# Kernel tuning notes

Hardware: AMD Instinct MI355X
Metric: run time of the kernel (lower is better)

The kernel has to match this reference:

```python
import jax, jax.numpy as jnp
import numpy as np

B, S, NX, H = 8, 1024, 1024, 16
HD = NX // H  # head dim = 64
MASKED_BIAS = -10000.0


def setup_inputs() -> dict:
    key = jax.random.key(0)
    ks = jax.random.split(key, 6)
    return {
        "x": jax.random.normal(ks[0], (B, S, NX), dtype=jnp.float32),
        "query": jax.random.normal(ks[1], (B, S, NX), dtype=jnp.float32),
        "c_attn_w": jax.random.normal(ks[2], (NX, 3 * NX), dtype=jnp.float32) * 0.02,
        "c_attn_b": jnp.zeros((3 * NX,), dtype=jnp.float32),
        "c_proj_w": jax.random.normal(ks[3], (NX, NX), dtype=jnp.float32) * 0.02,
        "c_proj_b": jnp.zeros((NX,), dtype=jnp.float32),
    }


def _split_heads(t):
    # [B, S, NX] -> [B, H, S, HD]
    b, s, _ = t.shape
    return t.reshape(b, s, H, HD).transpose(0, 2, 1, 3)


def reference(x, query, c_attn_w, c_attn_b, c_proj_w, c_proj_b):
    # Conv1D: y = x @ W + b
    kv = x @ c_attn_w + c_attn_b          # [B,S,3NX]; use key/value slices
    qy = query @ c_attn_w + c_attn_b      # [B,S,3NX]; use query slice
    q = _split_heads(qy[..., :NX])                     # [B,H,S,HD]
    k = _split_heads(kv[..., NX:2 * NX])               # [B,H,S,HD]
    v = _split_heads(kv[..., 2 * NX:])                 # [B,H,S,HD]

    w = jnp.einsum("bhqd,bhkd->bhqk", q, k) / jnp.sqrt(jnp.float32(HD))
    causal = jnp.tril(jnp.ones((S, S), dtype=bool))[None, None]
    w = jnp.where(causal, w, jnp.float32(MASKED_BIAS))
    w = jax.nn.softmax(w, axis=-1)
    a = jnp.einsum("bhqk,bhkd->bhqd", w, v)            # [B,H,S,HD]
    a = a.transpose(0, 2, 1, 3).reshape(B, S, NX)      # merge heads
    return a @ c_proj_w + c_proj_b
```

## Files before the change

kernel.cpp:

```cpp
#include <hip/hip_runtime.h>
#include <cstdint>
#include <cstddef>

#define Bb   8
#define Ss   1024
#define NXx  1024
#define Hh   16
#define HDd  64
#define Mm   (Bb*Ss)

typedef __bf16 bf16x8 __attribute__((ext_vector_type(8)));
typedef float  f32x4  __attribute__((ext_vector_type(4)));

__device__ __forceinline__ unsigned short f2bf(float f) {
    union { float f; unsigned int u; } v; v.f = f;
    return (unsigned short)((v.u + 0x8000u) >> 16);
}
__device__ __forceinline__ unsigned int f2bf_hi(float f) {
    union { float f; unsigned int u; } v; v.f = f;
    return (v.u + 0x8000u) & 0xffff0000u;
}

__device__ __forceinline__ void load_lds16(const unsigned short* g, unsigned short* lds_base) {
    __builtin_amdgcn_global_load_lds(
        (const __attribute__((address_space(1))) void*)g,
        (__attribute__((address_space(3))) void*)lds_base, 16, 0, 0);
}

__global__ __launch_bounds__(256) void prep(
    const float* __restrict__ x, const float* __restrict__ query,
    const float* __restrict__ caw, const float* __restrict__ cpw,
    unsigned short* __restrict__ xb, unsigned short* __restrict__ qb,
    unsigned short* __restrict__ Wt, unsigned short* __restrict__ Pt)
{
    __shared__ float tile[32][33];
    const int bid = blockIdx.x;
    const int tid = threadIdx.x;

    if (bid < 16384) {
        const float* in = (bid < 8192) ? x : query;
        unsigned short* out = (bid < 8192) ? xb : qb;
        const int i = ((bid & 8191) * 256 + tid) * 4;
        const float4 v = *(const float4*)(in + i);
        unsigned long long p = (unsigned long long)f2bf(v.x)
            | ((unsigned long long)f2bf(v.y) << 16)
            | ((unsigned long long)f2bf(v.z) << 32)
            | ((unsigned long long)f2bf(v.w) << 48);
        *(unsigned long long*)(out + i) = p;
        return;
    }

    const float* in;
    unsigned short* out;
    int C, t;
    if (bid < 16384 + 3072) { in = caw; out = Wt; C = 3072; t = bid - 16384; }
    else                    { in = cpw; out = Pt; C = 1024; t = bid - 19456; }
    const int ntx = C >> 5;
    const int c0 = (t % ntx) * 32, r0 = (t / ntx) * 32;
    const int tx = tid & 31, ty = tid >> 5;
    for (int i = ty; i < 32; i += 8)
        tile[i][tx] = in[(size_t)(r0 + i) * C + c0 + tx];
    __syncthreads();
    for (int i = ty; i < 32; i += 8)
        out[(size_t)(c0 + i) * 1024 + r0 + tx] = f2bf(tile[tx][i]);
}

__global__ __launch_bounds__(256) void gemm128(
    const unsigned short* __restrict__ Ax,
    const unsigned short* __restrict__ Aq,
    const unsigned short* __restrict__ Bt,
    const float* __restrict__ bias,
    int K, int mode,
    unsigned short* __restrict__ out_q,
    unsigned short* __restrict__ out_k,
    unsigned short* __restrict__ out_v,
    float* __restrict__ out_f)
{
    __shared__ unsigned short smem[16384];
    unsigned short (*As)[64] = (unsigned short (*)[64])(smem);
    unsigned short (*Bs)[64] = (unsigned short (*)[64])(smem + 8192);

    const int tid  = threadIdx.x;
    const int w    = tid >> 6;
    const int lane = tid & 63;

    const int nx   = (mode == 0) ? 24 : 8;
    const int nxh  = nx >> 1;
    const int n    = blockIdx.x;
    const int xcd  = n & 7;
    const int sgrp = n >> 3;
    const int m0   = ((xcd >> 1) * 16 + sgrp / nxh) * 128;
    const int n0   = ((xcd & 1) * nxh + sgrp % nxh) * 128;
    const int region = n0 >> 10;
    const unsigned short* A = (mode == 0 && region == 0) ? Aq : Ax;

    const int wm   = (w >> 1) * 64;
    const int wn   = (w & 1) * 64;
    const int lrow = lane & 15;
    const int quad = lane >> 4;

    f32x4 acc[4][4] = {};

    const int rr   = lane >> 3;
    const int scol = (((lane & 7) ^ (lane >> 3)) << 3);
    const unsigned short* Ag = A  + (size_t)(m0 + w * 32 + rr) * K + scol;
    const unsigned short* Bg = Bt + (size_t)(n0 + w * 32 + rr) * K + scol;
    unsigned short* ldsA = smem + (w * 32) * 64;
    unsigned short* ldsB = smem + 8192 + (w * 32) * 64;

    const int swz = lrow & 7;

    for (int k0 = 0; k0 < K; k0 += 64) {
        __syncthreads();
#pragma unroll
        for (int c = 0; c < 4; ++c) {
            load_lds16(Ag + (size_t)(c * 8) * K + k0, ldsA + c * 512);
            load_lds16(Bg + (size_t)(c * 8) * K + k0, ldsB + c * 512);
        }
        __syncthreads();
#pragma unroll
        for (int kk = 0; kk < 2; ++kk) {
            bf16x8 af[4], bfr[4];
            const int pc = (((kk * 4 + quad) ^ swz) << 3);
#pragma unroll
            for (int i = 0; i < 4; ++i) {
                af[i]  = *(const bf16x8*)&As[wm + i * 16 + lrow][pc];
                bfr[i] = *(const bf16x8*)&Bs[wn + i * 16 + lrow][pc];
            }
#pragma unroll
            for (int i = 0; i < 4; ++i)
#pragma unroll
                for (int j = 0; j < 4; ++j)
                    acc[i][j] = __builtin_amdgcn_mfma_f32_16x16x32_bf16(af[i], bfr[j], acc[i][j], 0, 0, 0);
        }
    }

    __syncthreads();

    if (mode == 1) {
#pragma unroll
        for (int i = 0; i < 4; ++i)
#pragma unroll
            for (int j = 0; j < 4; ++j) {
                const int ncol = n0 + wn + j * 16 + lrow;
                const float bv = bias[ncol];
#pragma unroll
                for (int r = 0; r < 4; ++r) {
                    const int mrow = m0 + wm + i * 16 + quad * 4 + r;
                    out_f[(size_t)mrow * NXx + ncol] = acc[i][j][r] + bv;
                }
            }
        return;
    }

    unsigned short* ep = smem + w * 2048;

    if (region != 2) {
        unsigned short* outp = (region == 0) ? out_q : out_k;
#pragma unroll
        for (int j = 0; j < 4; ++j) {
            const float bv = bias[n0 + wn + j * 16 + lrow];
#pragma unroll
            for (int i = 0; i < 4; ++i)
#pragma unroll
                for (int r = 0; r < 4; ++r)
                    ep[(i * 16 + quad * 4 + r) * 24 + lrow] = f2bf(acc[i][j][r] + bv);
#pragma unroll
            for (int t = 0; t < 2; ++t) {
                const int c    = t * 64 + lane;
                const int row  = c >> 1, ch = (c & 1) * 8;
                const int mrow = m0 + wm + row;
                const int cc   = (n0 + wn + j * 16 + ch) & (NXx - 1);
                const int hh   = cc >> 6, dd = cc & 63;
                const int bh   = (mrow >> 10) * Hh + hh;
                const int ss   = mrow & (Ss - 1);
                *(uint4*)&outp[((size_t)bh * Ss + ss) * HDd + dd] =
                    *(const uint4*)&ep[row * 24 + ch];
            }
        }
    } else {
#pragma unroll
        for (int j = 0; j < 4; ++j) {
            const float bv = bias[n0 + wn + j * 16 + lrow];
#pragma unroll
            for (int i = 0; i < 4; ++i)
#pragma unroll
                for (int r = 0; r < 4; ++r)
                    ep[lrow * 72 + i * 16 + quad * 4 + r] = f2bf(acc[i][j][r] + bv);
#pragma unroll
            for (int t = 0; t < 2; ++t) {
                const int c    = t * 64 + lane;
                const int col  = c >> 3, rc = (c & 7) * 8;
                const int cc   = (n0 + wn + j * 16 + col) & (NXx - 1);
                const int hh   = cc >> 6, dd = cc & 63;
                const int mrow = m0 + wm + rc;
                const int bh   = (mrow >> 10) * Hh + hh;
                const int ss   = mrow & (Ss - 1);
                *(uint4*)&out_v[((size_t)bh * HDd + dd) * Ss + ss] =
                    *(const uint4*)&ep[col * 72 + rc];
            }
        }
    }
}

__global__ __launch_bounds__(256) void flash_attn(
    const unsigned short* __restrict__ Qh,
    const unsigned short* __restrict__ Kh,
    const unsigned short* __restrict__ Vt,
    unsigned short* __restrict__ about)
{
    __shared__ unsigned short Ks[64][64];
    __shared__ unsigned short Vs[64][64];
    __shared__ unsigned short Pl[4][32][72];

    const int tid  = threadIdx.x;
    const int w    = tid >> 6;
    const int lane = tid & 63;
    const int bh   = blockIdx.x & 127;
    const int pr   = blockIdx.x >> 7;
    const int b    = bh >> 4, h = bh & 15;
    const int lrow = lane & 15;
    const int quad = lane >> 4;

    const unsigned short* Qb = Qh + (size_t)bh * Ss * HDd;
    const unsigned short* Kb = Kh + (size_t)bh * Ss * HDd;
    const unsigned short* Vb = Vt + (size_t)bh * HDd * Ss;

    const int sr = lane >> 3;
    const int lc = (((lane & 7) ^ (lane >> 3)) << 3);
    unsigned short* ldsK0 = &Ks[w * 16][0];
    unsigned short* ldsK1 = &Ks[w * 16 + 8][0];
    unsigned short* ldsV0 = &Vs[w * 16][0];
    unsigned short* ldsV1 = &Vs[w * 16 + 8][0];

    const int swz = lrow & 7;
    const int ca = ((quad ^ swz) << 3);
    const int cb = (((4 + quad) ^ swz) << 3);

    for (int half = 0; half < 2; ++half) {
        const int qt = half ? (7 - pr) : pr;
        const int qw = qt * 128 + w * 32;

        bf16x8 aq[2][2];
#pragma unroll
        for (int g = 0; g < 2; ++g)
#pragma unroll
            for (int c = 0; c < 2; ++c)
                aq[g][c] = *(const bf16x8*)(Qb + (size_t)(qw + g * 16 + lrow) * HDd + c * 32 + quad * 8);

        f32x4 O[2][4] = {};
        float lsum[2] = { 0.f, 0.f };

        const int nkt = 2 * qt + 2;
        for (int kt = 0; kt < nkt; ++kt) {
            const int k0 = kt * 64;

            __syncthreads();
            load_lds16(Kb + (size_t)(k0 + w * 16 + sr) * HDd + lc,     ldsK0);
            load_lds16(Kb + (size_t)(k0 + w * 16 + sr + 8) * HDd + lc, ldsK1);
            load_lds16(Vb + (size_t)(w * 16 + sr) * Ss + k0 + lc,      ldsV0);
            load_lds16(Vb + (size_t)(w * 16 + sr + 8) * Ss + k0 + lc,  ldsV1);
            __syncthreads();

            if (k0 > qw + 31) continue;

            f32x4 st[2][4] = {};
#pragma unroll
            for (int j = 0; j < 4; ++j) {
                const bf16x8 kf0 = *(const bf16x8*)&Ks[j * 16 + lrow][ca];
                const bf16x8 kf1 = *(const bf16x8*)&Ks[j * 16 + lrow][cb];
                st[0][j] = __builtin_amdgcn_mfma_f32_16x16x32_bf16(kf0, aq[0][0], st[0][j], 0, 0, 0);
                st[0][j] = __builtin_amdgcn_mfma_f32_16x16x32_bf16(kf1, aq[0][1], st[0][j], 0, 0, 0);
                st[1][j] = __builtin_amdgcn_mfma_f32_16x16x32_bf16(kf0, aq[1][0], st[1][j], 0, 0, 0);
                st[1][j] = __builtin_amdgcn_mfma_f32_16x16x32_bf16(kf1, aq[1][1], st[1][j], 0, 0, 0);
            }

            const bool needMask = (k0 + 63 > qw);
#pragma unroll
            for (int g = 0; g < 2; ++g) {
                const int qg = qw + g * 16 + lrow;
#pragma unroll
                for (int j = 0; j < 4; ++j) {
                    const int kbase = k0 + j * 16 + quad * 4;
                    float e0 = __expf(st[g][j][0] * 0.125f);
                    float e1 = __expf(st[g][j][1] * 0.125f);
                    float e2 = __expf(st[g][j][2] * 0.125f);
                    float e3 = __expf(st[g][j][3] * 0.125f);
                    if (needMask) {
                        if (kbase     > qg) e0 = 0.f;
                        if (kbase + 1 > qg) e1 = 0.f;
                        if (kbase + 2 > qg) e2 = 0.f;
                        if (kbase + 3 > qg) e3 = 0.f;
                    }
                    lsum[g] += (e0 + e1) + (e2 + e3);
                    uint2 pk;
                    pk.x = (unsigned)f2bf(e0) | f2bf_hi(e1);
                    pk.y = (unsigned)f2bf(e2) | f2bf_hi(e3);
                    *(uint2*)&Pl[w][g * 16 + lrow][j * 16 + quad * 4] = pk;
                }
            }

            bf16x8 ap[2][2];
#pragma unroll
            for (int g = 0; g < 2; ++g)
#pragma unroll
                for (int c = 0; c < 2; ++c)
                    ap[g][c] = *(const bf16x8*)&Pl[w][g * 16 + lrow][c * 32 + quad * 8];
#pragma unroll
            for (int f = 0; f < 4; ++f) {
                const bf16x8 vf0 = *(const bf16x8*)&Vs[f * 16 + lrow][ca];
                const bf16x8 vf1 = *(const bf16x8*)&Vs[f * 16 + lrow][cb];
                O[0][f] = __builtin_amdgcn_mfma_f32_16x16x32_bf16(ap[0][0], vf0, O[0][f], 0, 0, 0);
                O[0][f] = __builtin_amdgcn_mfma_f32_16x16x32_bf16(ap[0][1], vf1, O[0][f], 0, 0, 0);
                O[1][f] = __builtin_amdgcn_mfma_f32_16x16x32_bf16(ap[1][0], vf0, O[1][f], 0, 0, 0);
                O[1][f] = __builtin_amdgcn_mfma_f32_16x16x32_bf16(ap[1][1], vf1, O[1][f], 0, 0, 0);
            }
        }

#pragma unroll
        for (int g = 0; g < 2; ++g) {
            float l = lsum[g];
            l += __shfl_xor(l, 16);
            l += __shfl_xor(l, 32);
            const float inv = 1.0f / l;
#pragma unroll
            for (int r = 0; r < 4; ++r) {
                const float invr = __shfl(inv, quad * 4 + r);
                const int q = qw + g * 16 + quad * 4 + r;
                const size_t base = ((size_t)b * Ss + q) * NXx + h * HDd;
#pragma unroll
                for (int f = 0; f < 4; ++f)
                    about[base + f * 16 + lrow] = f2bf(O[g][f][r] * invr);
            }
        }
    }
}

extern "C" void kernel_launch(void* const* d_in, const int* in_sizes, int n_in,
                              void* d_out, int out_size, void* d_ws, size_t ws_size,
                              hipStream_t stream) {
    const float* x        = (const float*)d_in[0];
    const float* query    = (const float*)d_in[1];
    const float* c_attn_w = (const float*)d_in[2];
    const float* c_attn_b = (const float*)d_in[3];
    const float* c_proj_w = (const float*)d_in[4];
    const float* c_proj_b = (const float*)d_in[5];
    float* out = (float*)d_out;

    const size_t nTok = (size_t)Mm * NXx;
    char* ws = (char*)d_ws;
    unsigned short* xb    = (unsigned short*)ws;                 ws += nTok * 2;
    unsigned short* qb    = (unsigned short*)ws;                 ws += nTok * 2;
    unsigned short* Wt    = (unsigned short*)ws;                 ws += (size_t)3 * NXx * NXx * 2;
    unsigned short* Pt    = (unsigned short*)ws;                 ws += (size_t)NXx * NXx * 2;
    unsigned short* Qh    = (unsigned short*)ws;                 ws += nTok * 2;
    unsigned short* Kh    = (unsigned short*)ws;                 ws += nTok * 2;
    unsigned short* Vt    = (unsigned short*)ws;                 ws += nTok * 2;
    unsigned short* about = (unsigned short*)ws;                 ws += nTok * 2;
    if ((size_t)(ws - (char*)d_ws) > ws_size) return;

    prep<<<20480, 256, 0, stream>>>(x, query, c_attn_w, c_proj_w, xb, qb, Wt, Pt);

    gemm128<<<dim3(24 * 64), 256, 0, stream>>>(xb, qb, Wt, c_attn_b, NXx, 0,
                                               Qh, Kh, Vt, nullptr);
    flash_attn<<<512, 256, 0, stream>>>(Qh, Kh, Vt, about);

    gemm128<<<dim3(8 * 64), 256, 0, stream>>>(about, nullptr, Pt, c_proj_b, NXx, 1,
                                              nullptr, nullptr, nullptr, out);
}
```

Measured before the change: 265.6 us.

## Replace QKV projection GEMM with 256x256-tile, 8-wave pipelined kernel

Adds a gemm256 kernel that computes the fused QKV projection with 256x256 output tiles, 512 threads and double-buffered LDS loads interleaved with MFMA phases using barriers and s_setprio. It also remaps block indices so each XCD works on a contiguous group of tiles. The goal is more operand reuse per byte loaded and better overlap of global-to-LDS traffic with matrix math. The cost is higher register and LDS pressure (128 KB LDS per block) and only 384 blocks, which may leave some CUs underfilled.

```diff
diff --git a/kernel.cpp b/kernel.cpp
--- a/kernel.cpp
+++ b/kernel.cpp
@@ -198,6 +198,213 @@
                 const int ss   = mrow & (Ss - 1);
                 *(uint4*)&out_v[((size_t)bh * HDd + dd) * Ss + ss] =
                     *(const uint4*)&ep[col * 72 + rc];
+            }
+        }
+    }
+}
+
+__global__ __launch_bounds__(512, 2) void gemm256(
+    const unsigned short* __restrict__ Ax,
+    const unsigned short* __restrict__ Aq,
+    const unsigned short* __restrict__ Bt,
+    const float* __restrict__ bias,
+    unsigned short* __restrict__ out_q,
+    unsigned short* __restrict__ out_k,
+    unsigned short* __restrict__ out_v)
+{
+    __shared__ unsigned short lds[65536];
+
+    const int tid  = threadIdx.x;
+    const int w    = tid >> 6;
+    const int lane = tid & 63;
+    const int wm   = w >> 2;
+    const int wn   = w & 3;
+    const int lrow = lane & 15;
+    const int quad = lane >> 4;
+    const int swz  = lrow & 7;
+    const int ca   = (quad ^ swz) << 3;
+    const int cb   = ((4 + quad) ^ swz) << 3;
+
+    const int n    = blockIdx.x;
+    const int xcd  = n & 7;
+    const int sg   = n >> 3;
+    const int mi   = (xcd >> 1) * 8 + (sg & 7);
+    const int ni   = (xcd & 1) * 6 + (sg >> 3);
+    const int m0   = mi << 8;
+    const int n0   = ni << 8;
+    const int region = n0 >> 10;
+    const unsigned short* A = (region == 0) ? Aq : Ax;
+
+    const int srow = lane >> 3;
+    const int chnk = (((lane & 7) ^ srow) << 3);
+    const unsigned short* pA0 = A  + (size_t)(m0 +       w * 8 + srow) * 1024 + chnk;
+    const unsigned short* pA1 = A  + (size_t)(m0 +  64 + w * 8 + srow) * 1024 + chnk;
+    const unsigned short* pA2 = A  + (size_t)(m0 + 128 + w * 8 + srow) * 1024 + chnk;
+    const unsigned short* pA3 = A  + (size_t)(m0 + 192 + w * 8 + srow) * 1024 + chnk;
+    const unsigned short* pB0 = Bt + (size_t)(n0 +       w * 8 + srow) * 1024 + chnk;
+    const unsigned short* pB1 = Bt + (size_t)(n0 +  64 + w * 8 + srow) * 1024 + chnk;
+    const unsigned short* pB2 = Bt + (size_t)(n0 + 128 + w * 8 + srow) * 1024 + chnk;
+    const unsigned short* pB3 = Bt + (size_t)(n0 + 192 + w * 8 + srow) * 1024 + chnk;
+    const int wl = w * 512;
+
+    f32x4 acc[8][4] = {};
+
+    load_lds16(pA0, lds + 0 * 4096 + wl);
+    load_lds16(pA2, lds + 2 * 4096 + wl);
+    load_lds16(pB0, lds + 16384 + 0 * 4096 + wl);
+    load_lds16(pB1, lds + 16384 + 1 * 4096 + wl);
+    load_lds16(pB2, lds + 16384 + 2 * 4096 + wl);
+    load_lds16(pB3, lds + 16384 + 3 * 4096 + wl);
+    load_lds16(pA1, lds + 1 * 4096 + wl);
+    load_lds16(pA3, lds + 3 * 4096 + wl);
+    pA0 += 64; pA1 += 64; pA2 += 64; pA3 += 64;
+    pB0 += 64; pB1 += 64; pB2 += 64; pB3 += 64;
+
+    asm volatile("s_waitcnt vmcnt(2)" ::: "memory");
+    __builtin_amdgcn_s_barrier();
+    asm volatile("" ::: "memory");
+
+#pragma unroll 1
+    for (int t = 0; t < 16; ++t) {
+        const int as = (t & 1) << 15;
+        const int us = ((t & 1) ^ 1) << 15;
+        const bool st = (t < 15);
+        const int rbA = as + (wm * 128 + lrow) * 64;
+        const int rbB = as + 16384 + (wn * 64 + lrow) * 64;
+
+        bf16x8 a0f[4], a1f[4], b0q[4], b1q[4];
+
+#pragma unroll
+        for (int i = 0; i < 4; ++i) a0f[i] = *(const bf16x8*)&lds[rbA + i * 1024 + ca];
+#pragma unroll
+        for (int j = 0; j < 4; ++j) b0q[j] = *(const bf16x8*)&lds[rbB + j * 1024 + ca];
+        if (st) {
+            load_lds16(pA0, lds + us + 0 * 4096 + wl);
+            load_lds16(pA2, lds + us + 2 * 4096 + wl);
+            load_lds16(pB0, lds + us + 16384 + 0 * 4096 + wl);
+        }
+        __builtin_amdgcn_s_barrier();
+        asm volatile("s_waitcnt lgkmcnt(0)" ::: "memory");
+        __builtin_amdgcn_s_setprio(1);
+#pragma unroll
+        for (int i = 0; i < 4; ++i)
+#pragma unroll
+            for (int j = 0; j < 4; ++j)
+                acc[i][j] = __builtin_amdgcn_mfma_f32_16x16x32_bf16(a0f[i], b0q[j], acc[i][j], 0, 0, 0);
+        __builtin_amdgcn_s_setprio(0);
+        asm volatile("" ::: "memory");
+        __builtin_amdgcn_s_barrier();
+        asm volatile("" ::: "memory");
+
+#pragma unroll
+        for (int i = 0; i < 4; ++i) a1f[i] = *(const bf16x8*)&lds[rbA + i * 1024 + cb];
+#pragma unroll
+        for (int j = 0; j < 4; ++j) b1q[j] = *(const bf16x8*)&lds[rbB + j * 1024 + cb];
+        if (st) {
+            load_lds16(pB1, lds + us + 16384 + 1 * 4096 + wl);
+            load_lds16(pB2, lds + us + 16384 + 2 * 4096 + wl);
+            load_lds16(pB3, lds + us + 16384 + 3 * 4096 + wl);
+        }
+        __builtin_amdgcn_s_barrier();
+        asm volatile("s_waitcnt lgkmcnt(0)" ::: "memory");
+        __builtin_amdgcn_s_setprio(1);
+#pragma unroll
+        for (int i = 0; i < 4; ++i)
+#pragma unroll
+            for (int j = 0; j < 4; ++j)
+                acc[i][j] = __builtin_amdgcn_mfma_f32_16x16x32_bf16(a1f[i], b1q[j], acc[i][j], 0, 0, 0);
+        __builtin_amdgcn_s_setprio(0);
+        if (st) asm volatile("s_waitcnt vmcnt(6)" ::: "memory");
+        else    asm volatile("s_waitcnt vmcnt(0)" ::: "memory");
+        asm volatile("" ::: "memory");
+        __builtin_amdgcn_s_barrier();
+        asm volatile("" ::: "memory");
+
+#pragma unroll
+        for (int i = 0; i < 4; ++i) a0f[i] = *(const bf16x8*)&lds[rbA + 4096 + i * 1024 + ca];
+        __builtin_amdgcn_s_barrier();
+        asm volatile("s_waitcnt lgkmcnt(0)" ::: "memory");
+        __builtin_amdgcn_s_setprio(1);
+#pragma unroll
+        for (int i = 0; i < 4; ++i)
+#pragma unroll
+            for (int j = 0; j < 4; ++j)
+                acc[4 + i][j] = __builtin_amdgcn_mfma_f32_16x16x32_bf16(a0f[i], b0q[j], acc[4 + i][j], 0, 0, 0);
+        __builtin_amdgcn_s_setprio(0);
+        asm volatile("" ::: "memory");
+        __builtin_amdgcn_s_barrier();
+        asm volatile("" ::: "memory");
+
+#pragma unroll
+        for (int i = 0; i < 4; ++i) a1f[i] = *(const bf16x8*)&lds[rbA + 4096 + i * 1024 + cb];
+        if (st) {
+            load_lds16(pA1, lds + us + 1 * 4096 + wl);
+            load_lds16(pA3, lds + us + 3 * 4096 + wl);
+            pA0 += 64; pA1 += 64; pA2 += 64; pA3 += 64;
+            pB0 += 64; pB1 += 64; pB2 += 64; pB3 += 64;
+        }
+        __builtin_amdgcn_s_barrier();
+        asm volatile("s_waitcnt lgkmcnt(0)" ::: "memory");
+        __builtin_amdgcn_s_setprio(1);
+#pragma unroll
+        for (int i = 0; i < 4; ++i)
+#pragma unroll
+            for (int j = 0; j < 4; ++j)
+                acc[4 + i][j] = __builtin_amdgcn_mfma_f32_16x16x32_bf16(a1f[i], b1q[j], acc[4 + i][j], 0, 0, 0);
+        __builtin_amdgcn_s_setprio(0);
+        if (st) asm volatile("s_waitcnt vmcnt(2)" ::: "memory");
+        asm volatile("" ::: "memory");
+        __builtin_amdgcn_s_barrier();
+        asm volatile("" ::: "memory");
+    }
+
+    __syncthreads();
+
+    unsigned short* ep = lds + w * 8192;
+
+    if (region != 2) {
+        unsigned short* outp = (region == 0) ? out_q : out_k;
+#pragma unroll
+        for (int j = 0; j < 4; ++j) {
+            const float bv = bias[n0 + wn * 64 + j * 16 + lrow];
+#pragma unroll
+            for (int i = 0; i < 8; ++i)
+#pragma unroll
+                for (int r = 0; r < 4; ++r)
+                    ep[(i * 16 + quad * 4 + r) * 24 + lrow] = f2bf(acc[i][j][r] + bv);
+#pragma unroll
+            for (int tt = 0; tt < 4; ++tt) {
+                const int c    = tt * 64 + lane;
+                const int row  = c >> 1, ch = (c & 1) * 8;
+                const int mrow = m0 + wm * 128 + row;
+                const int cc   = (n0 + wn * 64 + j * 16 + ch) & (NXx - 1);
+                const int hh   = cc >> 6, dd = cc & 63;
+                const int bh   = (mrow >> 10) * Hh + hh;
+                const int ss   = mrow & (Ss - 1);
+                *(uint4*)&outp[((size_t)bh * Ss + ss) * HDd + dd] =
+                    *(const uint4*)&ep[row * 24 + ch];
+            }
+        }
+    } else {
+#pragma unroll
+        for (int j = 0; j < 4; ++j) {
+            const float bv = bias[n0 + wn * 64 + j * 16 + lrow];
+#pragma unroll
+            for (int i = 0; i < 8; ++i)
+#pragma unroll
+                for (int r = 0; r < 4; ++r)
+                    ep[lrow * 136 + i * 16 + quad * 4 + r] = f2bf(acc[i][j][r] + bv);
+#pragma unroll
+            for (int tt = 0; tt < 4; ++tt) {
+                const int c    = tt * 64 + lane;
+                const int col  = c >> 4, rc = (c & 15) * 8;
+                const int cc   = (n0 + wn * 64 + j * 16 + col) & (NXx - 1);
+                const int hh   = cc >> 6, dd = cc & 63;
+                const int mrow = m0 + wm * 128 + rc;
+                const int bh   = (mrow >> 10) * Hh + hh;
+                const int ss   = mrow & (Ss - 1);
+                *(uint4*)&out_v[((size_t)bh * HDd + dd) * Ss + ss] =
+                    *(const uint4*)&ep[col * 136 + rc];
             }
         }
     }
@@ -361,8 +568,8 @@
 
     prep<<<20480, 256, 0, stream>>>(x, query, c_attn_w, c_proj_w, xb, qb, Wt, Pt);
 
-    gemm128<<<dim3(24 * 64), 256, 0, stream>>>(xb, qb, Wt, c_attn_b, NXx, 0,
-                                               Qh, Kh, Vt, nullptr);
+    gemm256<<<384, 512, 0, stream>>>(xb, qb, Wt, c_attn_b, Qh, Kh, Vt);
+
     flash_attn<<<512, 256, 0, stream>>>(Qh, Kh, Vt, about);
 
     gemm128<<<dim3(8 * 64), 256, 0, stream>>>(about, nullptr, Pt, c_proj_b, NXx, 1,
```

After: 264.1 us. About the same (-0.6%).
